# Kernel tuning notes

Measured on AMD Instinct MI355X. Metric: run time of the kernel, lower is better.

The kernel has to match this reference:

```python
import jax, jax.numpy as jnp
import numpy as np

EPS = 1e-5


def _rmsnorm(x, eps=EPS):
    return x * jax.lax.rsqrt(jnp.mean(x * x, axis=-1, keepdims=True) + eps)


def _bitlinear(x, w):
    # fla-style BitLinear: RMSNorm (no affine) -> 8-bit activation quant (STE)
    # -> ternary weight quant (STE) -> linear. w is [out, in].
    xn = _rmsnorm(x)
    s = 127.0 / jnp.clip(jnp.max(jnp.abs(xn), axis=-1, keepdims=True), 1e-5, None)
    xq = jnp.clip(jnp.round(xn * s), -128.0, 127.0) / s
    xq = xn + jax.lax.stop_gradient(xq - xn)
    ws = 1.0 / jnp.clip(jnp.mean(jnp.abs(w)), 1e-5, None)
    wq = jnp.clip(jnp.round(w * ws), -1.0, 1.0) / ws
    wq = w + jax.lax.stop_gradient(wq - w)
    return jnp.einsum('bld,od->blo', xq, wq)


def _hgrn_scan(i, f):
    # h_t = f_t * h_{t-1} + i_t along axis=2 (seq), h_0 = 0.
    def combine(a, b):
        fa, ia = a
        fb, ib = b
        return fa * fb, ia * fb + ib
    _, h = jax.lax.associative_scan(combine, (f, i), axis=2)
    return h


def _forward(hidden_states, Wi, Wf, Wg, Wo, g_norm_weight, num_heads=1):
    b, l, d = hidden_states.shape
    i = _bitlinear(hidden_states, Wi)
    f = jax.nn.sigmoid(_bitlinear(hidden_states, Wf))
    i = jax.nn.silu(i) * (1.0 - f)  # swiglu(i, 1-f)
    # [b, l, (h d)] -> [b, h, l, d_head]
    i = i.reshape(b, l, num_heads, -1).transpose(0, 2, 1, 3)
    f = f.reshape(b, l, num_heads, -1).transpose(0, 2, 1, 3)
    h = _hgrn_scan(i, f)
    h = h.transpose(0, 2, 1, 3).reshape(b, l, d)
    # FusedRMSNormSwishGate: rmsnorm(g)*weight * h*sigmoid(h)
    g = _bitlinear(hidden_states, Wg)
    o = _rmsnorm(g) * g_norm_weight * (h * jax.nn.sigmoid(h))
    return _bitlinear(o, Wo)


def setup_inputs() -> dict:
    key = jax.random.key(0)
    ks = jax.random.split(key, 5)
    B, L, D = 4, 2048, 2048
    gain = 2 ** (-2.5) * (6.0 / (2 * D)) ** 0.5  # xavier_uniform with gain 2^-2.5
    def w(k):
        return jax.random.uniform(k, (D, D), jnp.float32, -gain, gain)
    return {
        'hidden_states': jax.random.normal(ks[0], (B, L, D), jnp.float32),
        'Wi': w(ks[1]),
        'Wf': w(ks[2]),
        'Wg': w(ks[3]),
        'Wo': w(ks[4]),
        'g_norm_weight': jnp.ones((D,), jnp.float32),
    }


def reference(hidden_states, Wi, Wf, Wg, Wo, g_norm_weight):
    return _forward(hidden_states, Wi, Wf, Wg, Wo, g_norm_weight)
```

## Files before the change

### kernel.cpp

```cpp
#include <hip/hip_runtime.h>
#include <stdint.h>

#define B_DIM 4
#define L_DIM 2048
#define D_DIM 2048
#define M_DIM 8192
#define K_DIM 2048
#define N_DIM 2048
#define WELEM (D_DIM * D_DIM)
#define CHUNK 32
#define NCH (L_DIM / CHUNK)

typedef int v4i __attribute__((ext_vector_type(4)));
typedef unsigned short bfraw;

#define AS1 __attribute__((address_space(1)))
#define AS3 __attribute__((address_space(3)))

__device__ __forceinline__ void gl_lds16(const void* g, void* l) {
    __builtin_amdgcn_global_load_lds((AS1 void*)g, (AS3 void*)l, 16, 0, 0);
}

__device__ __forceinline__ void wg_barrier() {
    asm volatile("" ::: "memory");
    __builtin_amdgcn_s_barrier();
    asm volatile("" ::: "memory");
}

__device__ __forceinline__ float sigmoidf_(float x) { return 1.0f / (1.0f + expf(-x)); }

__device__ __forceinline__ float bf2f(bfraw u) {
    union { unsigned int i; float f; } c; c.i = ((unsigned int)u) << 16; return c.f;
}
__device__ __forceinline__ bfraw f2bf(float f) {
    union { float f; unsigned int i; } c; c.f = f;
    unsigned int lsb = (c.i >> 16) & 1;
    c.i += 0x7fffu + lsb;
    return (bfraw)(c.i >> 16);
}

__device__ __forceinline__ void store_out(float* p, float v) { *p = v; }
__device__ __forceinline__ void store_out(bfraw* p, float v) { *p = f2bf(v); }

__device__ __forceinline__ float block_sum256(float v) {
#pragma unroll
    for (int off = 32; off > 0; off >>= 1) v += __shfl_down(v, off);
    __shared__ float sb[4];
    int lane = threadIdx.x & 63, wv = threadIdx.x >> 6;
    __syncthreads();
    if (lane == 0) sb[wv] = v;
    __syncthreads();
    return sb[0] + sb[1] + sb[2] + sb[3];
}

__device__ __forceinline__ void block_sum_max256(float& s, float& m) {
#pragma unroll
    for (int off = 32; off > 0; off >>= 1) {
        s += __shfl_down(s, off);
        m = fmaxf(m, __shfl_down(m, off));
    }
    __shared__ float sb2[8];
    int lane = threadIdx.x & 63, wv = threadIdx.x >> 6;
    __syncthreads();
    if (lane == 0) { sb2[wv] = s; sb2[4 + wv] = m; }
    __syncthreads();
    s = sb2[0] + sb2[1] + sb2[2] + sb2[3];
    m = fmaxf(fmaxf(sb2[4], sb2[5]), fmaxf(sb2[6], sb2[7]));
}

__global__ void wstats1(const float* __restrict__ w0, const float* __restrict__ w1,
                        const float* __restrict__ w2, const float* __restrict__ w3,
                        float* __restrict__ wpart) {
    int w = blockIdx.x >> 7;
    int slice = blockIdx.x & 127;
    const float* W = (w == 0) ? w0 : ((w == 1) ? w1 : ((w == 2) ? w2 : w3));
    const float4* p = (const float4*)(W + (size_t)slice * (WELEM / 128));
    float s = 0.f;
    for (int i = threadIdx.x; i < (WELEM / 128 / 4); i += 256) {
        float4 v = p[i];
        s += fabsf(v.x) + fabsf(v.y) + fabsf(v.z) + fabsf(v.w);
    }
    s = block_sum256(s);
    if (threadIdx.x == 0) wpart[blockIdx.x] = s;
}

__global__ void wstats2(const float* __restrict__ wpart, float* __restrict__ wdeq) {
    int w = threadIdx.x >> 6;
    int lane = threadIdx.x & 63;
    float s = wpart[w * 128 + lane] + wpart[w * 128 + 64 + lane];
#pragma unroll
    for (int off = 32; off > 0; off >>= 1) s += __shfl_down(s, off);
    if (lane == 0) wdeq[w] = fmaxf(s * (1.0f / (float)WELEM), 1e-5f);
}

__global__ void quant_all(const float* __restrict__ w0, const float* __restrict__ w1,
                          const float* __restrict__ w2, const float* __restrict__ w3,
                          const float* __restrict__ wdeq, int8_t* __restrict__ wq,
                          const float* __restrict__ x, int8_t* __restrict__ xq,
                          float* __restrict__ adeq) {
    if (blockIdx.x < 16384) {
        size_t idx = (size_t)blockIdx.x * 256 + threadIdx.x;
        int w = (int)(idx >> 20);
        size_t g = idx & ((1u << 20) - 1);
        const float* W = (w == 0) ? w0 : ((w == 1) ? w1 : ((w == 2) ? w2 : w3));
        float inv = 1.0f / wdeq[w];
        float4 v = ((const float4*)W)[g];
        int q0 = (int)rintf(v.x * inv); q0 = q0 < -1 ? -1 : (q0 > 1 ? 1 : q0);
        int q1 = (int)rintf(v.y * inv); q1 = q1 < -1 ? -1 : (q1 > 1 ? 1 : q1);
        int q2 = (int)rintf(v.z * inv); q2 = q2 < -1 ? -1 : (q2 > 1 ? 1 : q2);
        int q3 = (int)rintf(v.w * inv); q3 = q3 < -1 ? -1 : (q3 > 1 ? 1 : q3);
        uint32_t p = (uint32_t)(q0 & 0xff) | ((uint32_t)(q1 & 0xff) << 8) |
                     ((uint32_t)(q2 & 0xff) << 16) | ((uint32_t)(q3 & 0xff) << 24);
        ((uint32_t*)(wq + (size_t)w * WELEM))[g] = p;
        return;
    }
    int row = blockIdx.x - 16384, tid = threadIdx.x;
    const float4* xr = (const float4*)(x + (size_t)row * D_DIM);
    float4 a = xr[2 * tid], b = xr[2 * tid + 1];
    float v[8] = {a.x, a.y, a.z, a.w, b.x, b.y, b.z, b.w};
    float ss = 0.f, mx = 0.f;
#pragma unroll
    for (int j = 0; j < 8; j++) { ss += v[j] * v[j]; mx = fmaxf(mx, fabsf(v[j])); }
    block_sum_max256(ss, mx);
    float inv = rsqrtf(ss * (1.0f / (float)D_DIM) + 1e-5f);
    float anc = fmaxf(mx * inv, 1e-5f);
    float s = 127.0f / anc;
    if (tid == 0) adeq[row] = anc * (1.0f / 127.0f);
    float sc = inv * s;
    int q[8];
#pragma unroll
    for (int j = 0; j < 8; j++) {
        int t = (int)rintf(v[j] * sc);
        q[j] = t < -128 ? -128 : (t > 127 ? 127 : t);
    }
    uint32_t lo = (uint32_t)(q[0] & 0xff) | ((uint32_t)(q[1] & 0xff) << 8) |
                  ((uint32_t)(q[2] & 0xff) << 16) | ((uint32_t)(q[3] & 0xff) << 24);
    uint32_t hi = (uint32_t)(q[4] & 0xff) | ((uint32_t)(q[5] & 0xff) << 8) |
                  ((uint32_t)(q[6] & 0xff) << 16) | ((uint32_t)(q[7] & 0xff) << 24);
    ((uint2*)(xq + (size_t)row * D_DIM))[tid] = make_uint2(lo, hi);
}

#define BM 128
#define BN 256
#define BKB 64

template <typename OutT>
__device__ __forceinline__ void gemm_core(
    const int8_t* __restrict__ A, const int8_t* __restrict__ Bw,
    const float* __restrict__ adeq, float wsc,
    int m0, int n0, OutT* __restrict__ Cout) {
    __shared__ int8_t sA[2][BM * BKB];
    __shared__ int8_t sB[2][BN * BKB];
    int lane = threadIdx.x & 63;
    int wv = threadIdx.x >> 6;
    int wm = (wv & 1) * 64;
    int wn = (wv >> 1) * 128;
    int qq = lane >> 4;
    int mr = lane & 15;

    const v4i vzero = {0, 0, 0, 0};
    v4i acc[4][8];
#pragma unroll
    for (int i = 0; i < 4; i++)
#pragma unroll
        for (int j = 0; j < 8; j++) acc[i][j] = vzero;

    const int8_t* Asrc = A + (size_t)(m0 + mr) * K_DIM + qq * 16;
    const int8_t* Bsrc = Bw + (size_t)(n0 + mr) * K_DIM + qq * 16;
    const int agrp = (wv & 1) * 4;
    const int bgrp = (wv >> 1) * 8;

#define STAGE(c, kt) do {                                                         \
    gl_lds16(Asrc + (size_t)(wv * 16) * K_DIM + (kt),        &sA[c][wv * 1024]);        \
    gl_lds16(Asrc + (size_t)(64 + wv * 16) * K_DIM + (kt),   &sA[c][(4 + wv) * 1024]);  \
    gl_lds16(Bsrc + (size_t)(wv * 16) * K_DIM + (kt),        &sB[c][wv * 1024]);        \
    gl_lds16(Bsrc + (size_t)(64 + wv * 16) * K_DIM + (kt),   &sB[c][(4 + wv) * 1024]);  \
    gl_lds16(Bsrc + (size_t)(128 + wv * 16) * K_DIM + (kt),  &sB[c][(8 + wv) * 1024]);  \
    gl_lds16(Bsrc + (size_t)(192 + wv * 16) * K_DIM + (kt),  &sB[c][(12 + wv) * 1024]); \
  } while (0)

    STAGE(0, 0);
    int cur = 0;
#pragma unroll 2
    for (int kt = 0; kt < K_DIM; kt += BKB) {
        if (kt + BKB < K_DIM) {
            STAGE(cur ^ 1, kt + BKB);
            asm volatile("s_waitcnt vmcnt(6)" ::: "memory");
        } else {
            asm volatile("s_waitcnt vmcnt(0)" ::: "memory");
        }
        wg_barrier();

        v4i afrag[4], bfrag[8];
#pragma unroll
        for (int i = 0; i < 4; i++)
            afrag[i] = *(const v4i*)(&sA[cur][(agrp + i) * 1024 + lane * 16]);
#pragma unroll
        for (int j = 0; j < 8; j++)
            bfrag[j] = *(const v4i*)(&sB[cur][(bgrp + j) * 1024 + lane * 16]);

        __builtin_amdgcn_s_setprio(1);
#pragma unroll
        for (int i = 0; i < 4; i++)
#pragma unroll
            for (int j = 0; j < 8; j++)
                acc[i][j] = __builtin_amdgcn_mfma_i32_16x16x64_i8(afrag[i], bfrag[j], acc[i][j], 0, 0, 0);
        __builtin_amdgcn_s_setprio(0);

        wg_barrier();
        cur ^= 1;
    }
#undef STAGE

    int cc = mr;
#pragma unroll
    for (int i = 0; i < 4; i++) {
#pragma unroll
        for (int r = 0; r < 4; r++) {
            int row = m0 + wm + i * 16 + qq * 4 + r;
            float rs = adeq[row] * wsc;
            OutT* crow = Cout + (size_t)row * N_DIM + n0 + wn + cc;
#pragma unroll
            for (int j = 0; j < 8; j++) store_out(crow + j * 16, (float)acc[i][j][r] * rs);
        }
    }
}

__global__ __launch_bounds__(256, 2) void gemm_ifg(
    const int8_t* __restrict__ xq, const int8_t* __restrict__ wq,
    const float* __restrict__ adeq, const float* __restrict__ wdeq,
    bfraw* __restrict__ bufI, bfraw* __restrict__ bufF, bfraw* __restrict__ bufG) {
    int widx = blockIdx.x >> 3;
    int n0 = (blockIdx.x & 7) * BN;
    int m0 = blockIdx.y * BM;
    bfraw* outp = (widx == 0) ? bufI : ((widx == 1) ? bufF : bufG);
    gemm_core<bfraw>(xq, wq + (size_t)widx * WELEM, adeq, wdeq[widx], m0, n0, outp);
}

__global__ __launch_bounds__(256, 2) void gemm_o(
    const int8_t* __restrict__ oq, const int8_t* __restrict__ wq,
    const float* __restrict__ odeq, const float* __restrict__ wdeq,
    float* __restrict__ out) {
    gemm_core<float>(oq, wq + 3 * (size_t)WELEM, odeq, wdeq[3], blockIdx.y * BM,
                     blockIdx.x * BN, out);
}

__global__ void scan1(const bfraw* __restrict__ iL, const bfraw* __restrict__ fL,
                      float* __restrict__ Fc, float* __restrict__ Ic) {
    int idx = blockIdx.x * 256 + threadIdx.x;
    int d = idx & (D_DIM - 1);
    int c = (idx >> 11) & (NCH - 1);
    int b = idx >> 17;
    size_t base = ((size_t)(b * L_DIM + c * CHUNK)) * D_DIM + d;
    float F = 1.f, h = 0.f;
#pragma unroll 4
    for (int t = 0; t < CHUNK; t++) {
        float fr = bf2f(fL[base + (size_t)t * D_DIM]);
        float ir = bf2f(iL[base + (size_t)t * D_DIM]);
        float fv = sigmoidf_(fr);
        float iv = ir * sigmoidf_(ir) * (1.0f - fv);
        h = fv * h + iv;
        F *= fv;
    }
    size_t ci = ((size_t)b * NCH + c) * D_DIM + d;
    Fc[ci] = F;
    Ic[ci] = h;
}

__global__ void scan2(const float* __restrict__ Fc, const float* __restrict__ Ic,
                      float* __restrict__ Hc) {
    int idx = blockIdx.x * 256 + threadIdx.x;
    int d = idx & (D_DIM - 1);
    int b = idx >> 11;
    float h = 0.f;
    for (int c0 = 0; c0 < NCH; c0 += 8) {
        float F[8], I[8];
#pragma unroll
        for (int j = 0; j < 8; j++) {
            size_t ci = ((size_t)b * NCH + c0 + j) * D_DIM + d;
            F[j] = Fc[ci];
            I[j] = Ic[ci];
        }
#pragma unroll
        for (int j = 0; j < 8; j++) {
            size_t ci = ((size_t)b * NCH + c0 + j) * D_DIM + d;
            Hc[ci] = h;
            h = F[j] * h + I[j];
        }
    }
}

__global__ void scan3(const bfraw* __restrict__ iL, const bfraw* __restrict__ fL,
                      const float* __restrict__ Hc, bfraw* __restrict__ hout) {
    int idx = blockIdx.x * 256 + threadIdx.x;
    int d = idx & (D_DIM - 1);
    int c = (idx >> 11) & (NCH - 1);
    int b = idx >> 17;
    size_t base = ((size_t)(b * L_DIM + c * CHUNK)) * D_DIM + d;
    float h = Hc[((size_t)b * NCH + c) * D_DIM + d];
#pragma unroll 4
    for (int t = 0; t < CHUNK; t++) {
        size_t a = base + (size_t)t * D_DIM;
        float fr = bf2f(fL[a]);
        float ir = bf2f(iL[a]);
        float fv = sigmoidf_(fr);
        float iv = ir * sigmoidf_(ir) * (1.0f - fv);
        h = fv * h + iv;
        hout[a] = f2bf(h);
    }
}

union BF8 { uint4 u; bfraw s[8]; };

__global__ void gout_quant(const bfraw* __restrict__ gL, const bfraw* __restrict__ h,
                           const float* __restrict__ gw, int8_t* __restrict__ oq,
                           float* __restrict__ odeq) {
    int row = blockIdx.x, tid = threadIdx.x;
    BF8 g8, h8;
    g8.u = ((const uint4*)(gL + (size_t)row * D_DIM))[tid];
    float gv[8];
    float ss = 0.f;
#pragma unroll
    for (int j = 0; j < 8; j++) { gv[j] = bf2f(g8.s[j]); ss += gv[j] * gv[j]; }
    float ssg = block_sum256(ss);
    float invg = rsqrtf(ssg * (1.0f / (float)D_DIM) + 1e-5f);

    h8.u = ((const uint4*)(h + (size_t)row * D_DIM))[tid];
    const float4* wr = (const float4*)gw;
    float4 w0 = wr[2 * tid], w1 = wr[2 * tid + 1];
    float wv[8] = {w0.x, w0.y, w0.z, w0.w, w1.x, w1.y, w1.z, w1.w};
    float o[8];
    float sso = 0.f, amax = 0.f;
#pragma unroll
    for (int j = 0; j < 8; j++) {
        float hv = bf2f(h8.s[j]);
        o[j] = gv[j] * invg * wv[j] * hv * sigmoidf_(hv);
        sso += o[j] * o[j];
        amax = fmaxf(amax, fabsf(o[j]));
    }
    block_sum_max256(sso, amax);
    float invo = rsqrtf(sso * (1.0f / (float)D_DIM) + 1e-5f);
    float anc = fmaxf(amax * invo, 1e-5f);
    float s = 127.0f / anc;
    if (tid == 0) odeq[row] = anc * (1.0f / 127.0f);
    float sc = invo * s;
    int q[8];
#pragma unroll
    for (int j = 0; j < 8; j++) {
        int t = (int)rintf(o[j] * sc);
        q[j] = t < -128 ? -128 : (t > 127 ? 127 : t);
    }
    uint32_t lo = (uint32_t)(q[0] & 0xff) | ((uint32_t)(q[1] & 0xff) << 8) |
                  ((uint32_t)(q[2] & 0xff) << 16) | ((uint32_t)(q[3] & 0xff) << 24);
    uint32_t hi = (uint32_t)(q[4] & 0xff) | ((uint32_t)(q[5] & 0xff) << 8) |
                  ((uint32_t)(q[6] & 0xff) << 16) | ((uint32_t)(q[7] & 0xff) << 24);
    ((uint2*)(oq + (size_t)row * D_DIM))[tid] = make_uint2(lo, hi);
}

extern "C" void kernel_launch(void* const* d_in, const int* in_sizes, int n_in,
                              void* d_out, int out_size, void* d_ws, size_t ws_size,
                              hipStream_t stream) {
    const float* x  = (const float*)d_in[0];
    const float* Wi = (const float*)d_in[1];
    const float* Wf = (const float*)d_in[2];
    const float* Wg = (const float*)d_in[3];
    const float* Wo = (const float*)d_in[4];
    const float* gw = (const float*)d_in[5];
    float* out = (float*)d_out;

    char* ws = (char*)d_ws;
    float*  wdeq  = (float*)(ws + 0);
    float*  wpart = (float*)(ws + 256);
    float*  adeq  = (float*)(ws + 0x10000);
    float*  odeq  = (float*)(ws + 0x20000);
    int8_t* xq    = (int8_t*)(ws + 0x100000);
    int8_t* wq    = (int8_t*)(ws + 0x1100000);
    float*  Fc    = (float*)(ws + 0x2100000);
    float*  Ic    = (float*)(ws + 0x2300000);
    float*  Hc    = (float*)(ws + 0x2500000);
    bfraw*  bufI  = (bfraw*)(ws + 0x4000000);
    bfraw*  bufF  = (bfraw*)(ws + 0x6000000);
    bfraw*  bufG  = (bfraw*)(ws + 0x8000000);
    bfraw*  hbuf  = (bfraw*)(ws + 0xA000000);

    wstats1<<<512, 256, 0, stream>>>(Wi, Wf, Wg, Wo, wpart);
    wstats2<<<1, 256, 0, stream>>>(wpart, wdeq);
    quant_all<<<16384 + 8192, 256, 0, stream>>>(Wi, Wf, Wg, Wo, wdeq, wq, x, xq, adeq);

    gemm_ifg<<<dim3(24, M_DIM / BM), 256, 0, stream>>>(xq, wq, adeq, wdeq, bufI, bufF, bufG);

    scan1<<<2048, 256, 0, stream>>>(bufI, bufF, Fc, Ic);
    scan2<<<32, 256, 0, stream>>>(Fc, Ic, Hc);
    scan3<<<2048, 256, 0, stream>>>(bufI, bufF, Hc, hbuf);

    gout_quant<<<M_DIM, 256, 0, stream>>>(bufG, hbuf, gw, xq , odeq);
    gemm_o<<<dim3(N_DIM / BN, M_DIM / BM), 256, 0, stream>>>(xq , wq, odeq, wdeq, out);

    (void)in_sizes; (void)n_in; (void)out_size; (void)ws_size;
}
```

Baseline: 477.4 us.

## Switch int8 GEMM to 32x32x32 MFMA with prefetch-two pipeline and interleaved LDS reads

```diff
diff --git a/kernel.cpp b/kernel.cpp
--- a/kernel.cpp
+++ b/kernel.cpp
@@ -11,7 +11,8 @@
 #define CHUNK 32
 #define NCH (L_DIM / CHUNK)
 
-typedef int v4i __attribute__((ext_vector_type(4)));
+typedef int v4i  __attribute__((ext_vector_type(4)));
+typedef int v16i __attribute__((ext_vector_type(16)));
 typedef unsigned short bfraw;
 
 #define AS1 __attribute__((address_space(1)))
@@ -144,84 +145,104 @@
 #define BN 256
 #define BKB 64
 
+#define MFMA32(a, b, c) __builtin_amdgcn_mfma_i32_32x32x32_i8((a), (b), (c), 0, 0, 0)
+
 template <typename OutT>
 __device__ __forceinline__ void gemm_core(
     const int8_t* __restrict__ A, const int8_t* __restrict__ Bw,
     const float* __restrict__ adeq, float wsc,
     int m0, int n0, OutT* __restrict__ Cout) {
-    __shared__ int8_t sA[2][BM * BKB];
-    __shared__ int8_t sB[2][BN * BKB];
+    __shared__ __align__(16) int8_t sA[2][BM * BKB];
+    __shared__ __align__(16) int8_t sB[2][BN * BKB];
     int lane = threadIdx.x & 63;
     int wv = threadIdx.x >> 6;
     int wm = (wv & 1) * 64;
     int wn = (wv >> 1) * 128;
-    int qq = lane >> 4;
-    int mr = lane & 15;
-
-    const v4i vzero = {0, 0, 0, 0};
-    v4i acc[4][8];
-#pragma unroll
-    for (int i = 0; i < 4; i++)
-#pragma unroll
-        for (int j = 0; j < 8; j++) acc[i][j] = vzero;
-
-    const int8_t* Asrc = A + (size_t)(m0 + mr) * K_DIM + qq * 16;
-    const int8_t* Bsrc = Bw + (size_t)(n0 + mr) * K_DIM + qq * 16;
-    const int agrp = (wv & 1) * 4;
-    const int bgrp = (wv >> 1) * 8;
-
-#define STAGE(c, kt) do {                                                         \
-    gl_lds16(Asrc + (size_t)(wv * 16) * K_DIM + (kt),        &sA[c][wv * 1024]);        \
-    gl_lds16(Asrc + (size_t)(64 + wv * 16) * K_DIM + (kt),   &sA[c][(4 + wv) * 1024]);  \
-    gl_lds16(Bsrc + (size_t)(wv * 16) * K_DIM + (kt),        &sB[c][wv * 1024]);        \
-    gl_lds16(Bsrc + (size_t)(64 + wv * 16) * K_DIM + (kt),   &sB[c][(4 + wv) * 1024]);  \
-    gl_lds16(Bsrc + (size_t)(128 + wv * 16) * K_DIM + (kt),  &sB[c][(8 + wv) * 1024]);  \
-    gl_lds16(Bsrc + (size_t)(192 + wv * 16) * K_DIM + (kt),  &sB[c][(12 + wv) * 1024]); \
+    int r32 = lane & 31;
+    int h32 = lane >> 5;
+
+    const v16i vzero = {0, 0, 0, 0, 0, 0, 0, 0, 0, 0, 0, 0, 0, 0, 0, 0};
+    v16i acc[2][4];
+#pragma unroll
+    for (int m = 0; m < 2; m++)
+#pragma unroll
+        for (int j = 0; j < 4; j++) acc[m][j] = vzero;
+
+    const int8_t* Asrc = A + (size_t)(m0 + r32) * K_DIM + h32 * 16;
+    const int8_t* Bsrc = Bw + (size_t)(n0 + r32) * K_DIM + h32 * 16;
+    const int ag = (wv & 1) * 2;
+    const int bg = (wv >> 1) * 4;
+
+#define STAGE(c, kt) do {                                                                  \
+    gl_lds16(Asrc + (size_t)(wv * 32) * K_DIM + (kt),            &sA[c][wv * 2048]);        \
+    gl_lds16(Asrc + (size_t)(wv * 32) * K_DIM + (kt) + 32,       &sA[c][wv * 2048 + 1024]); \
+    gl_lds16(Bsrc + (size_t)(wv * 32) * K_DIM + (kt),            &sB[c][wv * 2048]);        \
+    gl_lds16(Bsrc + (size_t)(wv * 32) * K_DIM + (kt) + 32,       &sB[c][wv * 2048 + 1024]); \
+    gl_lds16(Bsrc + (size_t)((4 + wv) * 32) * K_DIM + (kt),      &sB[c][(4 + wv) * 2048]);  \
+    gl_lds16(Bsrc + (size_t)((4 + wv) * 32) * K_DIM + (kt) + 32, &sB[c][(4 + wv) * 2048 + 1024]); \
   } while (0)
 
     STAGE(0, 0);
+    STAGE(1, BKB);
+    asm volatile("s_waitcnt vmcnt(6)" ::: "memory");
+    wg_barrier();
+
     int cur = 0;
 #pragma unroll 2
     for (int kt = 0; kt < K_DIM; kt += BKB) {
+        v4i af[2][2], bf[4][2];
+#pragma unroll
+        for (int m = 0; m < 2; m++)
+#pragma unroll
+            for (int k = 0; k < 2; k++)
+                af[m][k] = *(const v4i*)(&sA[cur][(ag + m) * 2048 + k * 1024 + lane * 16]);
+        bf[0][0] = *(const v4i*)(&sB[cur][bg * 2048 + lane * 16]);
+        bf[0][1] = *(const v4i*)(&sB[cur][bg * 2048 + 1024 + lane * 16]);
+
+#pragma unroll
+        for (int j = 0; j < 3; j++) {
+            bf[j + 1][0] = *(const v4i*)(&sB[cur][(bg + j + 1) * 2048 + lane * 16]);
+            bf[j + 1][1] = *(const v4i*)(&sB[cur][(bg + j + 1) * 2048 + 1024 + lane * 16]);
+            asm volatile("s_waitcnt lgkmcnt(2)" ::: "memory");
+            __builtin_amdgcn_sched_barrier(0);
+            __builtin_amdgcn_s_setprio(1);
+            acc[0][j] = MFMA32(af[0][0], bf[j][0], acc[0][j]);
+            acc[1][j] = MFMA32(af[1][0], bf[j][0], acc[1][j]);
+            acc[0][j] = MFMA32(af[0][1], bf[j][1], acc[0][j]);
+            acc[1][j] = MFMA32(af[1][1], bf[j][1], acc[1][j]);
+            __builtin_amdgcn_s_setprio(0);
+        }
+        asm volatile("s_waitcnt lgkmcnt(0)" ::: "memory");
+        __builtin_amdgcn_sched_barrier(0);
+        wg_barrier();
+        if (kt + 2 * BKB < K_DIM) STAGE(cur, kt + 2 * BKB);
+        __builtin_amdgcn_s_setprio(1);
+        acc[0][3] = MFMA32(af[0][0], bf[3][0], acc[0][3]);
+        acc[1][3] = MFMA32(af[1][0], bf[3][0], acc[1][3]);
+        acc[0][3] = MFMA32(af[0][1], bf[3][1], acc[0][3]);
+        acc[1][3] = MFMA32(af[1][1], bf[3][1], acc[1][3]);
+        __builtin_amdgcn_s_setprio(0);
         if (kt + BKB < K_DIM) {
-            STAGE(cur ^ 1, kt + BKB);
-            asm volatile("s_waitcnt vmcnt(6)" ::: "memory");
-        } else {
-            asm volatile("s_waitcnt vmcnt(0)" ::: "memory");
+            if (kt + 2 * BKB < K_DIM)
+                asm volatile("s_waitcnt vmcnt(6)" ::: "memory");
+            else
+                asm volatile("s_waitcnt vmcnt(0)" ::: "memory");
+            wg_barrier();
         }
-        wg_barrier();
-
-        v4i afrag[4], bfrag[8];
-#pragma unroll
-        for (int i = 0; i < 4; i++)
-            afrag[i] = *(const v4i*)(&sA[cur][(agrp + i) * 1024 + lane * 16]);
-#pragma unroll
-        for (int j = 0; j < 8; j++)
-            bfrag[j] = *(const v4i*)(&sB[cur][(bgrp + j) * 1024 + lane * 16]);
-
-        __builtin_amdgcn_s_setprio(1);
-#pragma unroll
-        for (int i = 0; i < 4; i++)
-#pragma unroll
-            for (int j = 0; j < 8; j++)
-                acc[i][j] = __builtin_amdgcn_mfma_i32_16x16x64_i8(afrag[i], bfrag[j], acc[i][j], 0, 0, 0);
-        __builtin_amdgcn_s_setprio(0);
-
-        wg_barrier();
         cur ^= 1;
     }
 #undef STAGE
 
-    int cc = mr;
-#pragma unroll
-    for (int i = 0; i < 4; i++) {
-#pragma unroll
-        for (int r = 0; r < 4; r++) {
-            int row = m0 + wm + i * 16 + qq * 4 + r;
+#pragma unroll
+    for (int m = 0; m < 2; m++) {
+#pragma unroll
+        for (int r = 0; r < 16; r++) {
+            int rr = (r & 3) + 8 * (r >> 2) + 4 * h32;
+            int row = m0 + wm + m * 32 + rr;
             float rs = adeq[row] * wsc;
-            OutT* crow = Cout + (size_t)row * N_DIM + n0 + wn + cc;
-#pragma unroll
-            for (int j = 0; j < 8; j++) store_out(crow + j * 16, (float)acc[i][j][r] * rs);
+            OutT* crow = Cout + (size_t)row * N_DIM + n0 + wn + r32;
+#pragma unroll
+            for (int j = 0; j < 4; j++) store_out(crow + j * 32, (float)acc[m][j][r] * rs);
         }
     }
 }
```

After: 482.4 us. Within noise of the previous version (+1.0%).
